# Performance work log

Measured on AMD Instinct MI355X. Metric: run time of the kernel, lower is better.

## Reference

```python
import jax, jax.numpy as jnp
import numpy as np

N, E, D_IN, D_OUT, SIZE = 50000, 800000, 128, 128, 4
NEG_SLOPE = 0.01  # torch leaky_relu default


def setup_inputs() -> dict:
    key = jax.random.key(0)
    k1, k2, k3, k4, k5 = jax.random.split(key, 5)
    x = jax.random.normal(k1, (N, D_IN), dtype=jnp.float32)
    edge_index = jax.random.randint(k2, (2, E), 0, N, dtype=jnp.int32)
    s = 1.0 / np.sqrt(D_IN)
    W_l = jax.random.uniform(k3, (SIZE, D_IN, D_OUT), jnp.float32, -s, s)
    W_r = jax.random.uniform(k4, (SIZE, D_IN, D_OUT), jnp.float32, -s, s)
    b = jax.random.uniform(k5, (SIZE, D_OUT), jnp.float32, -s, s)
    return {"x": x, "edge_index": edge_index, "W_l": W_l, "W_r": W_r, "b": b}


def reference(x, edge_index, W_l, W_r, b):
    src, dst = edge_index[0], edge_index[1]
    # mean aggregation of source features into destination nodes (shared by all heads)
    agg = jax.ops.segment_sum(x[src], dst, num_segments=N)          # [N, D_IN]
    cnt = jax.ops.segment_sum(jnp.ones((E, 1), x.dtype), dst, num_segments=N)
    mean_nbr = agg / jnp.maximum(cnt, 1.0)
    # per-head SAGEConv: lin_l(mean_nbr) + lin_r(x) + b, batched over heads
    h = (jnp.einsum('nd,sdo->nso', mean_nbr, W_l)
         + jnp.einsum('nd,sdo->nso', x, W_r)
         + b[None, :, :])                                           # [N, SIZE, D_OUT]
    h = jnp.where(h > 0, h, NEG_SLOPE * h)                          # leaky_relu
    return h.reshape(N, SIZE * D_OUT)                               # concat over heads
```

## Files before the change

kernel.cpp:

```cpp
#include <hip/hip_runtime.h>

#define NN    50000
#define NE    800000
#define DIN   128
#define NH    4
#define NEG   0.01f
#define NROWS 50048
#define NBKT  1024
#define BD    49
#define NBLK  391
#define EPB   2048
#define NXBF  3128
#define EBUF  2048
#define QS    21.166666667f
#define QSI   0.047244094f

typedef __attribute__((ext_vector_type(8))) short short8v;
typedef __attribute__((ext_vector_type(8))) ushort ushort8v;
typedef __attribute__((ext_vector_type(4))) float float4v;

__device__ __forceinline__ ushort f2bf(float f) {
    union { float f; unsigned u; } c; c.f = f;
    unsigned u = c.u;
    return (ushort)((u + 0x7FFFu + ((u >> 16) & 1u)) >> 16);
}

__global__ __launch_bounds__(256) void k_init(int* __restrict__ cursor) {
    for (int i = threadIdx.x; i < NBKT; i += 256) cursor[i] = i * EBUF;
}

__global__ __launch_bounds__(256) void k_work(const float* __restrict__ x,
                                              const float* __restrict__ Wl,
                                              const float* __restrict__ Wr,
                                              const int* __restrict__ ei,
                                              ushort* __restrict__ A,
                                              unsigned* __restrict__ xq,
                                              ushort* __restrict__ Bt,
                                              int* __restrict__ cursor,
                                              unsigned* __restrict__ ebkt) {
    __shared__ int h[NBKT];
    __shared__ int lcur[NBKT];
    const int bid = blockIdx.x, t = threadIdx.x;
    if (bid < NBLK) {
        const int blk = bid;
        for (int i = t; i < NBKT; i += 256) h[i] = 0;
        __syncthreads();
        const int base = blk * EPB;
        int dsts[8], srcs[8];
        #pragma unroll
        for (int i = 0; i < 8; ++i) {
            const int e = base + i * 256 + t;
            if (e < NE) {
                dsts[i] = ei[NE + e];
                srcs[i] = ei[e];
                atomicAdd(&h[dsts[i] / BD], 1);
            }
        }
        __syncthreads();
        for (int i = t; i < NBKT; i += 256) {
            const int c = h[i];
            lcur[i] = c ? atomicAdd(&cursor[i], c) : 0;
        }
        __syncthreads();
        #pragma unroll
        for (int i = 0; i < 8; ++i) {
            const int e = base + i * 256 + t;
            if (e < NE) {
                const int b = dsts[i] / BD;
                const int r = atomicAdd(&lcur[b], 1);
                ebkt[r] = ((unsigned)dsts[i] << 16) | (unsigned)srcs[i];
            }
        }
    } else if (bid < NBLK + NXBF) {
        const int tid = (bid - NBLK) * 256 + t;
        const int n = tid >> 4, seg = tid & 15;
        ushort8v o;
        unsigned w0 = 0, w1 = 0;
        if (n < NN) {
            const float4* xp = (const float4*)(x + (size_t)n * DIN + seg * 8);
            float4 v0 = xp[0], v1 = xp[1];
            float v[8] = {v0.x, v0.y, v0.z, v0.w, v1.x, v1.y, v1.z, v1.w};
            unsigned q[8];
            #pragma unroll
            for (int i = 0; i < 8; ++i) {
                o[i] = f2bf(v[i]);
                int qi = (int)rintf(fminf(fmaxf(v[i] * QS, -127.f), 127.f));
                q[i] = (unsigned)qi & 0xFFu;
            }
            w0 = q[0] | (q[1] << 8) | (q[2] << 16) | (q[3] << 24);
            w1 = q[4] | (q[5] << 8) | (q[6] << 16) | (q[7] << 24);
        } else {
            #pragma unroll
            for (int i = 0; i < 8; ++i) o[i] = 0;
        }
        *(ushort8v*)(A + (size_t)n * 256 + 128 + seg * 8) = o;
        *(uint2*)(xq + (size_t)n * 32 + seg * 2) = make_uint2(w0, w1);
    } else {
        const int tid = (bid - NBLK - NXBF) * 256 + t;
        const int j = tid >> 5, kc = tid & 31;
        const int s = j >> 7, col = j & 127;
        short8v o;
        #pragma unroll
        for (int i = 0; i < 8; ++i) {
            int k = kc * 8 + i;
            float w = (k < 128) ? Wl[((size_t)s * DIN + k) * 128 + col]
                                : Wr[((size_t)s * DIN + (k - 128)) * 128 + col];
            o[i] = (short)f2bf(w);
        }
        *(short8v*)(Bt + (size_t)j * 256 + kc * 8) = o;
    }
}

#define ACC1(w, k)                              \
    {                                           \
        acc[(k) + 0] += (int)((w) << 24) >> 24; \
        acc[(k) + 1] += (int)((w) << 16) >> 24; \
        acc[(k) + 2] += (int)((w) << 8) >> 24;  \
        acc[(k) + 3] += (int)(w) >> 24;         \
    }
#define ACC4(v) { ACC1((v).x, 0) ACC1((v).y, 4) ACC1((v).z, 8) ACC1((v).w, 12) }

__global__ __launch_bounds__(512) void k_bg(const unsigned* __restrict__ ebkt,
                                            const int* __restrict__ cursor,
                                            const unsigned* __restrict__ xq,
                                            ushort* __restrict__ A) {
    __shared__ unsigned ebuf[EBUF];
    __shared__ ushort lsrc[EBUF];
    __shared__ int lcnt[BD], loff[BD], lcur[BD];
    const int t = threadIdx.x, b = blockIdx.x;
    const int d0 = b * BD;
    const int s0 = b * EBUF;
    int cnt = cursor[b] - s0;
    if (cnt > EBUF) cnt = EBUF;
    if (cnt < 0) cnt = 0;
    if (t < BD) { lcnt[t] = 0; lcur[t] = 0; }
    __syncthreads();
    for (int e = t; e < cnt; e += 512) {
        const unsigned u = ebkt[s0 + e];
        ebuf[e] = u;
        atomicAdd(&lcnt[(int)(u >> 16) - d0], 1);
    }
    __syncthreads();
    if (t == 0) {
        int run = 0;
        #pragma unroll
        for (int i = 0; i < BD; ++i) { loff[i] = run; run += lcnt[i]; }
    }
    __syncthreads();
    for (int e = t; e < cnt; e += 512) {
        const unsigned u = ebuf[e];
        const int dl = (int)(u >> 16) - d0;
        const int r = atomicAdd(&lcur[dl], 1);
        lsrc[loff[dl] + r] = (ushort)(u & 0xFFFFu);
    }
    __syncthreads();

    const int gl = t & 7;
    const int dl = t >> 3;
    if (dl < BD) {
        const int n = d0 + dl;
        if (n < NROWS) {
            const int deg = lcnt[dl], base = loff[dl];
            int acc[16];
            #pragma unroll
            for (int i = 0; i < 16; ++i) acc[i] = 0;
            int j = 0;
            for (; j + 8 <= deg; j += 8) {
                uint4 v0 = *(const uint4*)(xq + (size_t)lsrc[base + j] * 32 + gl * 4);
                uint4 v1 = *(const uint4*)(xq + (size_t)lsrc[base + j + 1] * 32 + gl * 4);
                uint4 v2 = *(const uint4*)(xq + (size_t)lsrc[base + j + 2] * 32 + gl * 4);
                uint4 v3 = *(const uint4*)(xq + (size_t)lsrc[base + j + 3] * 32 + gl * 4);
                uint4 v4 = *(const uint4*)(xq + (size_t)lsrc[base + j + 4] * 32 + gl * 4);
                uint4 v5 = *(const uint4*)(xq + (size_t)lsrc[base + j + 5] * 32 + gl * 4);
                uint4 v6 = *(const uint4*)(xq + (size_t)lsrc[base + j + 6] * 32 + gl * 4);
                uint4 v7 = *(const uint4*)(xq + (size_t)lsrc[base + j + 7] * 32 + gl * 4);
                ACC4(v0) ACC4(v1) ACC4(v2) ACC4(v3)
                ACC4(v4) ACC4(v5) ACC4(v6) ACC4(v7)
            }
            for (; j + 4 <= deg; j += 4) {
                uint4 v0 = *(const uint4*)(xq + (size_t)lsrc[base + j] * 32 + gl * 4);
                uint4 v1 = *(const uint4*)(xq + (size_t)lsrc[base + j + 1] * 32 + gl * 4);
                uint4 v2 = *(const uint4*)(xq + (size_t)lsrc[base + j + 2] * 32 + gl * 4);
                uint4 v3 = *(const uint4*)(xq + (size_t)lsrc[base + j + 3] * 32 + gl * 4);
                ACC4(v0) ACC4(v1) ACC4(v2) ACC4(v3)
            }
            for (; j < deg; ++j) {
                uint4 v = *(const uint4*)(xq + (size_t)lsrc[base + j] * 32 + gl * 4);
                ACC4(v)
            }
            const float invq = (n < NN) ? QSI / (float)(deg > 1 ? deg : 1) : 0.f;
            ushort8v o0, o1;
            #pragma unroll
            for (int i = 0; i < 8; ++i) o0[i] = f2bf((float)acc[i] * invq);
            #pragma unroll
            for (int i = 0; i < 8; ++i) o1[i] = f2bf((float)acc[8 + i] * invq);
            ushort* dst = A + (size_t)n * 256 + gl * 16;
            *(ushort8v*)dst = o0;
            *(ushort8v*)(dst + 8) = o1;
        }
    }
}

__global__ __launch_bounds__(256, 1) void k_mm(const ushort* __restrict__ A,
                                               const ushort* __restrict__ Bt,
                                               const float* __restrict__ bias,
                                               float* __restrict__ out)
{
    const int t = threadIdx.x;
    const int wid = t >> 6, l = t & 63;
    const int lr = l & 15;
    const int lk = l >> 4;

    const ushort* bt = Bt + (size_t)wid * 128 * 256;
    short8v b[8][8];
    #pragma unroll
    for (int kt = 0; kt < 8; ++kt)
        #pragma unroll
        for (int n = 0; n < 8; ++n)
            b[kt][n] = *(const short8v*)&bt[(size_t)(n * 16 + lr) * 256 + kt * 32 + lk * 8];

    float bcol[8];
    #pragma unroll
    for (int n = 0; n < 8; ++n) bcol[n] = bias[wid * 128 + n * 16 + lr];

    for (int rt = blockIdx.x; rt < NROWS / 32; rt += gridDim.x) {
        const int node0 = rt * 32;
        float4v acc[2][8];
        #pragma unroll
        for (int m = 0; m < 2; ++m)
            #pragma unroll
            for (int n = 0; n < 8; ++n)
                acc[m][n] = (float4v){0.f, 0.f, 0.f, 0.f};

        #pragma unroll
        for (int kt = 0; kt < 8; ++kt) {
            short8v af[2];
            #pragma unroll
            for (int m = 0; m < 2; ++m) {
                const int row = node0 + m * 16 + lr;
                af[m] = *(const short8v*)&A[(size_t)row * 256 + (kt * 4 + lk) * 8];
            }
            #pragma unroll
            for (int n = 0; n < 8; ++n)
                #pragma unroll
                for (int m = 0; m < 2; ++m)
                    acc[m][n] = __builtin_amdgcn_mfma_f32_16x16x32_bf16(af[m], b[kt][n], acc[m][n], 0, 0, 0);
        }

        #pragma unroll
        for (int m = 0; m < 2; ++m) {
            #pragma unroll
            for (int r = 0; r < 4; ++r) {
                const int node = node0 + m * 16 + lk * 4 + r;
                if (node < NN) {
                    float* op = out + (size_t)node * (NH * DIN) + wid * 128 + lr;
                    #pragma unroll
                    for (int n = 0; n < 8; ++n) {
                        float h = acc[m][n][r] + bcol[n];
                        op[n * 16] = h > 0.f ? h : NEG * h;
                    }
                }
            }
        }
    }
}

extern "C" void kernel_launch(void* const* d_in, const int* in_sizes, int n_in,
                              void* d_out, int out_size, void* d_ws, size_t ws_size,
                              hipStream_t stream) {
    const float* x  = (const float*)d_in[0];
    const int*   ei = (const int*)d_in[1];
    const float* Wl = (const float*)d_in[2];
    const float* Wr = (const float*)d_in[3];
    const float* b  = (const float*)d_in[4];
    float* out = (float*)d_out;

    ushort*   A      = (ushort*)d_ws;
    ushort*   Bt     = A + (size_t)NROWS * 256;
    unsigned* xq     = (unsigned*)(Bt + 512 * 256);
    unsigned* ebkt   = xq + (size_t)NROWS * 32;
    int*      cursor = (int*)(ebkt + (size_t)NBKT * EBUF);

    k_init<<<1, 256, 0, stream>>>(cursor);
    k_work<<<NBLK + NXBF + 64, 256, 0, stream>>>(x, Wl, Wr, ei, A, xq, Bt, cursor, ebkt);
    k_bg  <<<NBKT, 512, 0, stream>>>(ebkt, cursor, xq, A);
    k_mm  <<<256, 256, 0, stream>>>(A, Bt, b, out);
}
```

Baseline: 93.33 us.

## Double-buffer A tiles in LDS via async global_load_lds with XOR swizzle

The matmul kernel now prefetches the next 32-row bf16 A tile into a second shared-memory buffer with 16-byte global_load_lds instructions while the current tile is computed. The tile is read back from LDS through an XOR swizzle instead of straight from global memory. The aim is to hide global load latency behind the MFMA work and the output stores. The tile-loop stride is hardcoded to 256 rather than gridDim.x, so correctness depends on the launch using exactly 256 blocks. The extra barrier per tile adds some synchronisation cost.

Result: faster. 83.36 us, median of 2 (-10.7%).

```diff
diff --git a/kernel.cpp b/kernel.cpp
--- a/kernel.cpp
+++ b/kernel.cpp
@@ -206,10 +206,12 @@
                                                const float* __restrict__ bias,
                                                float* __restrict__ out)
 {
+    __shared__ ushort sA[2][32 * 256];
     const int t = threadIdx.x;
     const int wid = t >> 6, l = t & 63;
     const int lr = l & 15;
     const int lk = l >> 4;
+    const int chunk = l & 31;
 
     const ushort* bt = Bt + (size_t)wid * 128 * 256;
     short8v b[8][8];
@@ -223,7 +225,31 @@
     #pragma unroll
     for (int n = 0; n < 8; ++n) bcol[n] = bias[wid * 128 + n * 16 + lr];
 
-    for (int rt = blockIdx.x; rt < NROWS / 32; rt += gridDim.x) {
+    const int NT = NROWS / 32;
+
+#define STAGE(buf, tile)                                                        \
+    {                                                                           \
+        const int node0_ = (tile) * 32;                                         \
+        _Pragma("unroll")                                                       \
+        for (int inst = 0; inst < 4; ++inst) {                                  \
+            const int r0 = wid * 8 + inst * 2;                                  \
+            const int row = r0 + (l >> 5);                                      \
+            const ushort* src = A + (size_t)(node0_ + row) * 256                \
+                                  + ((chunk ^ (row & 7)) * 8);                  \
+            __builtin_amdgcn_global_load_lds(                                   \
+                (const __attribute__((address_space(1))) unsigned*)src,         \
+                (__attribute__((address_space(3))) unsigned*)&sA[buf][r0 * 256],\
+                16, 0, 0);                                                      \
+        }                                                                       \
+    }
+
+    int cur = 0;
+    STAGE(0, (int)blockIdx.x)
+    for (int rt = blockIdx.x; rt < NT; rt += 256) {
+        __syncthreads();
+        const int nxt = rt + 256;
+        if (nxt < NT) STAGE(cur ^ 1, nxt)
+
         const int node0 = rt * 32;
         float4v acc[2][8];
         #pragma unroll
@@ -237,8 +263,8 @@
             short8v af[2];
             #pragma unroll
             for (int m = 0; m < 2; ++m) {
-                const int row = node0 + m * 16 + lr;
-                af[m] = *(const short8v*)&A[(size_t)row * 256 + (kt * 4 + lk) * 8];
+                const int row = m * 16 + lr;
+                af[m] = *(const short8v*)&sA[cur][row * 256 + (((kt * 4 + lk) ^ (row & 7)) * 8)];
             }
             #pragma unroll
             for (int n = 0; n < 8; ++n)
@@ -262,7 +288,9 @@
                 }
             }
         }
-    }
+        cur ^= 1;
+    }
+#undef STAGE
 }
 
 extern "C" void kernel_launch(void* const* d_in, const int* in_sizes, int n_in,
```
